# Performance work log

Measured on AMD Instinct MI355X. Metric: run time of the kernel, lower is better.

The kernel has to match this reference:

```python
import jax, jax.numpy as jnp
import numpy as np

L, H = 3, 8
B, N, D, E = 4, 256, 128, 128
NH, EH1, EH2 = 512, 512, 512


def _ln(x, g, b):
    m = x.mean(-1, keepdims=True)
    v = ((x - m) ** 2).mean(-1, keepdims=True)
    return (x - m) * jax.lax.rsqrt(v + 1e-5) * g + b


def setup_inputs() -> dict:
    key = jax.random.key(0)
    ks = jax.random.split(key, 16)
    w = lambda k, *s: jax.random.normal(k, s, jnp.float32) * 0.02
    inp = {
        'node_features': jax.random.normal(ks[0], (B, N, D), jnp.float32),
        'edge_features': jax.random.normal(ks[1], (B, N, N, E), jnp.float32),
        'Wqkv_n': w(ks[2], L, D, 3 * D), 'bqkv_n': jnp.zeros((L, 3 * D)),
        'Wqkv_e': w(ks[3], L, E, 3 * D), 'bqkv_e': jnp.zeros((L, 3 * D)),
        'Wo': w(ks[4], L, D, D), 'bo': jnp.zeros((L, D)),
        'Wn1': w(ks[5], L, D, NH), 'bn1': jnp.zeros((L, NH)),
        'Wn2': w(ks[6], L, NH, D), 'bn2': jnp.zeros((L, D)),
        'ln1n_g': jnp.ones((L, D)), 'ln1n_b': jnp.zeros((L, D)),
        'ln2n_g': jnp.ones((L, D)), 'ln2n_b': jnp.zeros((L, D)),
        'We1a': w(ks[7], L, 2 * D + 2 * E, EH1), 'be1a': jnp.zeros((L, EH1)),
        'We1b': w(ks[8], L, EH1, E), 'be1b': jnp.zeros((L, E)),
        'We2a': w(ks[9], L, E, EH2), 'be2a': jnp.zeros((L, EH2)),
        'We2b': w(ks[10], L, EH2, E), 'be2b': jnp.zeros((L, E)),
        'ln1e_g': jnp.ones((L, E)), 'ln1e_b': jnp.zeros((L, E)),
        'ln2e_g': jnp.ones((L, E)), 'ln2e_b': jnp.zeros((L, E)),
    }
    return inp


def reference(node_features, edge_features, Wqkv_n, bqkv_n, Wqkv_e, bqkv_e, Wo, bo,
              Wn1, bn1, Wn2, bn2, ln1n_g, ln1n_b, ln2n_g, ln2n_b,
              We1a, be1a, We1b, be1b, We2a, be2a, We2b, be2b,
              ln1e_g, ln1e_b, ln2e_g, ln2e_b):
    n, e = node_features, edge_features
    b_, N_, D_ = n.shape
    hd = D_ // H
    scale = 1.0 / np.sqrt(hd).astype(np.float32)
    for l in range(Wqkv_n.shape[0]):
        # ---- edge-biased attention ----
        qkv_n = (n @ Wqkv_n[l] + bqkv_n[l]).reshape(b_, N_, H, 3 * hd).transpose(0, 2, 1, 3)  # B,H,N,3hd
        q_n, k_n, v_n = jnp.split(qkv_n, 3, axis=-1)
        qkv_e = (e @ Wqkv_e[l] + bqkv_e[l]).reshape(b_, N_, N_, H, 3 * hd).transpose(0, 3, 1, 2, 4)  # B,H,N,N,3hd
        q_e, k_e, v_e = jnp.split(qkv_e, 3, axis=-1)
        q = q_n[:, :, :, None, :] + q_e  # B,H,N,N,hd
        # NOTE: the original torch code overwrites k with q (`k = q.reshape(...)`),
        # so scores are the squared norm of q; k_n/k_e are dead code. Faithful.
        scores = jnp.einsum('bhijd,bhijd->bhij', q, q) * scale
        att = jax.nn.softmax(scores, axis=-1)
        v = v_n[:, :, None, :, :] + v_e  # B,H,N,N,hd
        out = jnp.einsum('bhij,bhijd->bhid', att, v)  # B,H,N,hd
        out = out.transpose(0, 2, 1, 3).reshape(b_, N_, D_) @ Wo[l] + bo[l]
        n = _ln(n + out, ln1n_g[l], ln1n_b[l])
        ff = jax.nn.relu(n @ Wn1[l] + bn1[l]) @ Wn2[l] + bn2[l]
        n = _ln(n + ff, ln2n_g[l], ln2n_b[l])
        # ---- edge update ----
        src = jnp.broadcast_to(n[:, None, :, :], (b_, N_, N_, D_))  # node j
        tgt = jnp.broadcast_to(n[:, :, None, :], (b_, N_, N_, D_))  # node i
        cat = jnp.concatenate([e, e.transpose(0, 2, 1, 3), src, tgt], axis=-1)
        e1 = jax.nn.relu(cat @ We1a[l] + be1a[l]) @ We1b[l] + be1b[l]
        e = _ln(e + e1, ln1e_g[l], ln1e_b[l])
        e2 = jax.nn.relu(e @ We2a[l] + be2a[l]) @ We2b[l] + be2b[l]
        e = _ln(e + e2, ln2e_g[l], ln2e_b[l])
    return n
```

## Files before the change

kernel.cpp:

```cpp
#include <hip/hip_runtime.h>

typedef unsigned short u16;
typedef __bf16 bf16x8 __attribute__((ext_vector_type(8)));
typedef float f32x4 __attribute__((ext_vector_type(4)));

#define NB 4
#define NN 256
#define DD 128
#define RNN 262144

__device__ __forceinline__ u16 f2b(float f) {
    unsigned u = __builtin_bit_cast(unsigned, f);
    unsigned rb = ((u >> 16) & 1u) + 0x7FFFu;
    return (u16)((u + rb) >> 16);
}
__device__ __forceinline__ float b2f(u16 u) {
    return __builtin_bit_cast(float, ((unsigned)u) << 16);
}

__device__ __forceinline__ void glds16(const void* g, void* l) {
    __builtin_amdgcn_global_load_lds((const __attribute__((address_space(1))) void*)g,
                                     (__attribute__((address_space(3))) void*)l, 16, 0, 0);
}

__global__ void prep_weights(const float* __restrict__ Wqkv_e, const float* __restrict__ bqkv_e,
                             const float* __restrict__ We1a, const float* __restrict__ We1b,
                             const float* __restrict__ We2a, const float* __restrict__ We2b,
                             u16* wqT, u16* wv, float* bqp, float* bvp,
                             u16* we1aT, u16* we1bT, u16* we2aT, u16* we2bT) {
    int l = blockIdx.z, sec = blockIdx.y;
    int idx = blockIdx.x * 256 + threadIdx.x;
    if (sec == 0) {
        if (idx < 16384) {
            int n = idx >> 7, k = idx & 127;
            int col = (n >> 4) * 48 + (n & 15);
            wqT[l * 16384 + n * 128 + k] = f2b(Wqkv_e[l * 49152 + k * 384 + col]);
        }
    } else if (sec == 1) {
        if (idx < 16384) {
            int k = idx >> 7, c = idx & 127;
            int col = (c >> 4) * 48 + 32 + (c & 15);
            wv[l * 16384 + k * 128 + c] = f2b(Wqkv_e[l * 49152 + k * 384 + col]);
        }
        if (idx < 128) {
            bqp[l * 128 + idx] = bqkv_e[l * 384 + (idx >> 4) * 48 + (idx & 15)];
            bvp[l * 128 + idx] = bqkv_e[l * 384 + (idx >> 4) * 48 + 32 + (idx & 15)];
        }
    } else if (sec == 2) {
        if (idx < 131072) {
            int n = idx >> 8, k = idx & 255;
            we1aT[l * 131072 + n * 256 + k] = f2b(We1a[l * 262144 + k * 512 + n]);
        }
    } else if (sec == 3) {
        if (idx < 65536) {
            int n = idx >> 9, k = idx & 511;
            we1bT[l * 65536 + n * 512 + k] = f2b(We1b[l * 65536 + k * 128 + n]);
        }
    } else if (sec == 4) {
        if (idx < 65536) {
            int n = idx >> 7, k = idx & 127;
            we2aT[l * 65536 + n * 128 + k] = f2b(We2a[l * 65536 + k * 512 + n]);
        }
    } else {
        if (idx < 65536) {
            int n = idx >> 9, k = idx & 511;
            we2bT[l * 65536 + n * 512 + k] = f2b(We2b[l * 65536 + k * 128 + n]);
        }
    }
}

__global__ void init_e(const float4* __restrict__ src, ushort4* __restrict__ dst) {
    const long n4 = 8388608;
    for (long i = (long)blockIdx.x * blockDim.x + threadIdx.x; i < n4; i += (long)gridDim.x * blockDim.x) {
        float4 v = src[i];
        ushort4 o;
        o.x = f2b(v.x); o.y = f2b(v.y); o.z = f2b(v.z); o.w = f2b(v.w);
        dst[i] = o;
    }
}

__global__ void init_n(const float* __restrict__ node, float* __restrict__ nf) {
    int i = blockIdx.x * 256 + threadIdx.x;
    if (i < 131072) nf[i] = node[i];
}

__launch_bounds__(512)
__global__ void pre_node_kernel(const float* __restrict__ nf, const float* __restrict__ We1a,
                                float* __restrict__ preS, float* __restrict__ preT) {
    __shared__ float nr[128];
    int tid = threadIdx.x;
    int row = blockIdx.x;
    if (tid < 128) nr[tid] = nf[(long)row * 128 + tid];
    __syncthreads();
    int c = tid;
    float s = 0.f, t = 0.f;
    const float* Ws = We1a + (long)256 * 512 + c;
    const float* Wt = We1a + (long)384 * 512 + c;
    #pragma unroll 8
    for (int k = 0; k < 128; ++k) {
        float nv = nr[k];
        s += nv * Ws[k * 512];
        t += nv * Wt[k * 512];
    }
    preS[(long)row * 512 + c] = s;
    preT[(long)row * 512 + c] = t;
}

__global__ void qkvn_kernel(const float* __restrict__ nf, const float* __restrict__ W,
                            const float* __restrict__ bias, float* __restrict__ qn, float* __restrict__ vn) {
    __shared__ float nr[128];
    int tid = threadIdx.x;
    int row = blockIdx.x;
    if (tid < 128) nr[tid] = nf[(long)row * 128 + tid];
    __syncthreads();
    int c = tid & 127;
    bool isq = tid < 128;
    int col = (c >> 4) * 48 + (c & 15) + (isq ? 0 : 32);
    float a = bias[col];
    #pragma unroll 8
    for (int k = 0; k < 128; ++k) a += nr[k] * W[k * 384 + col];
    if (isq) qn[(long)row * 128 + c] = a;
    else     vn[(long)row * 128 + c] = a;
}

__launch_bounds__(256, 2)
__global__ void scores_kernel(const u16* __restrict__ ein, const u16* __restrict__ WqT,
                              const float* __restrict__ bqp, const float* __restrict__ qn,
                              float* __restrict__ scoresp) {
    __shared__ u16 As[128 * 64];
    __shared__ u16 Bs[128 * 64];
    int tid = threadIdx.x;
    int wid = tid >> 6, lane = tid & 63;
    int bid = blockIdx.x;
    int jhalf = bid & 1, bi = bid >> 1;
    int b = bi >> 8, i = bi & 255;
    int wr = wid >> 1, wc = wid & 1;

    f32x4 acc[4][4];
    f32x4 z = {0.f, 0.f, 0.f, 0.f};
    #pragma unroll
    for (int m = 0; m < 4; ++m)
        #pragma unroll
        for (int n = 0; n < 4; ++n) acc[m][n] = z;

    const long arow0 = ((long)(b * NN + i) * NN + jhalf * 128);
    for (int kt = 0; kt < 2; ++kt) {
        int k0 = kt << 6;
        #pragma unroll
        for (int p = 0; p < 4; ++p) {
            int r = p * 32 + (tid >> 3);
            int ch = tid & 7;
            const u16* src = ein + (arow0 + r) * 128 + k0 + ((ch ^ (r & 7)) << 3);
            glds16(src, (char*)As + (p << 12) + (wid << 10));
            int n = p * 32 + (tid >> 3);
            const u16* bsrc = WqT + (long)n * 128 + k0 + ((ch ^ (n & 7)) << 3);
            glds16(bsrc, (char*)Bs + (p << 12) + (wid << 10));
        }
        __syncthreads();
        #pragma unroll
        for (int ks = 0; ks < 2; ++ks) {
            bf16x8 af[4], bfr[4];
            #pragma unroll
            for (int m = 0; m < 4; ++m) {
                int r = wr * 64 + m * 16 + (lane & 15);
                int ch = (ks * 4 + (lane >> 4)) ^ (r & 7);
                af[m] = *reinterpret_cast<const bf16x8*>(&As[r * 64 + ch * 8]);
            }
            #pragma unroll
            for (int n = 0; n < 4; ++n) {
                int c = wc * 64 + n * 16 + (lane & 15);
                int ch = (ks * 4 + (lane >> 4)) ^ (c & 7);
                bfr[n] = *reinterpret_cast<const bf16x8*>(&Bs[c * 64 + ch * 8]);
            }
            #pragma unroll
            for (int m = 0; m < 4; ++m)
                #pragma unroll
                for (int n = 0; n < 4; ++n)
                    acc[m][n] = __builtin_amdgcn_mfma_f32_16x16x32_bf16(af[m], bfr[n], acc[m][n], 0, 0, 0);
        }
        __syncthreads();
    }
    const float* qnb = qn + (long)(b * NN + i) * 128;
    #pragma unroll
    for (int m = 0; m < 4; ++m) {
        #pragma unroll
        for (int n = 0; n < 4; ++n) {
            int col = wc * 64 + n * 16 + (lane & 15);
            float add = bqp[col] + qnb[col];
            float sv[4];
            #pragma unroll
            for (int t = 0; t < 4; ++t) { float qv = acc[m][n][t] + add; sv[t] = qv * qv; }
            #pragma unroll
            for (int mk = 1; mk <= 8; mk <<= 1)
                #pragma unroll
                for (int t = 0; t < 4; ++t) sv[t] += __shfl_xor(sv[t], mk);
            if ((lane & 15) == 0) {
                int head = wc * 4 + n;
                int jb = jhalf * 128 + wr * 64 + m * 16 + ((lane >> 4) << 2);
                long sbase = ((long)(b * 8 + head) * 256 + i) * 256 + jb;
                #pragma unroll
                for (int t = 0; t < 4; ++t) scoresp[sbase + t] = sv[t] * 0.25f;
            }
        }
    }
}

__launch_bounds__(256)
__global__ void attn_pv_kernel(const float* __restrict__ scoresp, const u16* __restrict__ ein,
                               const float* __restrict__ vn, const u16* __restrict__ Wv,
                               const float* __restrict__ bvp, float* __restrict__ attn_o) {
    __shared__ float s_s[8 * 256];
    __shared__ float g_s[8 * 128];
    __shared__ float part[256];
    int tid = threadIdx.x;
    int b = blockIdx.x >> 8, i = blockIdx.x & 255;
    for (int v = tid; v < 2048; v += 256) {
        int h = v >> 8, j = v & 255;
        s_s[v] = scoresp[((long)(b * 8 + h) * 256 + i) * 256 + j];
    }
    __syncthreads();
    {
        int h = tid >> 5, lg = tid & 31;
        float vals[8], mx = -1e30f;
        #pragma unroll
        for (int t = 0; t < 8; ++t) { vals[t] = s_s[h * 256 + lg + t * 32]; mx = fmaxf(mx, vals[t]); }
        #pragma unroll
        for (int mk = 16; mk; mk >>= 1) mx = fmaxf(mx, __shfl_xor(mx, mk));
        float sum = 0.f;
        #pragma unroll
        for (int t = 0; t < 8; ++t) { vals[t] = __expf(vals[t] - mx); sum += vals[t]; }
        #pragma unroll
        for (int mk = 16; mk; mk >>= 1) sum += __shfl_xor(sum, mk);
        float inv = 1.f / sum;
        #pragma unroll
        for (int t = 0; t < 8; ++t) s_s[h * 256 + lg + t * 32] = vals[t] * inv;
    }
    __syncthreads();
    {
        int k = tid & 127, h0 = tid >> 7;
        const u16* erow = ein + ((long)(b * NN + i) * NN) * 128 + k;
        float a0 = 0, a1 = 0, a2 = 0, a3 = 0;
        for (int j = 0; j < 256; ++j) {
            float ev = b2f(erow[(long)j * 128]);
            a0 += s_s[(h0    ) * 256 + j] * ev;
            a1 += s_s[(h0 + 2) * 256 + j] * ev;
            a2 += s_s[(h0 + 4) * 256 + j] * ev;
            a3 += s_s[(h0 + 6) * 256 + j] * ev;
        }
        g_s[(h0    ) * 128 + k] = a0;
        g_s[(h0 + 2) * 128 + k] = a1;
        g_s[(h0 + 4) * 128 + k] = a2;
        g_s[(h0 + 6) * 128 + k] = a3;
    }
    __syncthreads();
    {
        int c = tid & 127, half = tid >> 7;
        int h = c >> 4;
        float a = 0.f;
        for (int j = half * 128; j < half * 128 + 128; ++j)
            a += s_s[h * 256 + j] * vn[((long)(b * NN + j)) * 128 + c];
        for (int k = half * 64; k < half * 64 + 64; ++k)
            a += g_s[h * 128 + k] * b2f(Wv[k * 128 + c]);
        part[tid] = a;
    }
    __syncthreads();
    if (tid < 128)
        attn_o[((long)(b * NN + i)) * 128 + tid] = part[tid] + part[128 + tid] + bvp[tid];
}

__launch_bounds__(256)
__global__ void node_kernel(const float* __restrict__ attn_o, float* __restrict__ nf,
                            const float* __restrict__ Wo, const float* __restrict__ bo,
                            const float* __restrict__ Wn1, const float* __restrict__ bn1,
                            const float* __restrict__ Wn2, const float* __restrict__ bn2,
                            const float* __restrict__ g1, const float* __restrict__ b1,
                            const float* __restrict__ g2, const float* __restrict__ b2) {
    __shared__ float ao[128], nr[128], n1[128], hb[512];
    __shared__ float red[8];
    int tid = threadIdx.x;
    int wid = tid >> 6, lane = tid & 63;
    long base = (long)blockIdx.x * 128;
    if (tid < 128) { ao[tid] = attn_o[base + tid]; nr[tid] = nf[base + tid]; }
    __syncthreads();
    float x = 0.f;
    if (tid < 128) {
        float a = bo[tid];
        #pragma unroll 8
        for (int k = 0; k < 128; ++k) a += ao[k] * Wo[k * 128 + tid];
        x = nr[tid] + a;
    }
    float s = (tid < 128) ? x : 0.f, q = (tid < 128) ? x * x : 0.f;
    #pragma unroll
    for (int mk = 1; mk <= 32; mk <<= 1) { s += __shfl_xor(s, mk); q += __shfl_xor(q, mk); }
    if (lane == 0) { red[wid * 2] = s; red[wid * 2 + 1] = q; }
    __syncthreads();
    float sum = red[0] + red[2] + red[4] + red[6];
    float sq  = red[1] + red[3] + red[5] + red[7];
    float mean = sum * (1.f / 128.f);
    float var = sq * (1.f / 128.f) - mean * mean;
    float rs = rsqrtf(var + 1e-5f);
    __syncthreads();
    if (tid < 128) n1[tid] = (x - mean) * rs * g1[tid] + b1[tid];
    __syncthreads();
    for (int c = tid; c < 512; c += 256) {
        float a = bn1[c];
        #pragma unroll 8
        for (int k = 0; k < 128; ++k) a += n1[k] * Wn1[k * 512 + c];
        hb[c] = a > 0.f ? a : 0.f;
    }
    __syncthreads();
    float y = 0.f;
    if (tid < 128) {
        float a = bn2[tid];
        #pragma unroll 8
        for (int k = 0; k < 512; ++k) a += hb[k] * Wn2[k * 128 + tid];
        y = n1[tid] + a;
    }
    float s2 = (tid < 128) ? y : 0.f, q2 = (tid < 128) ? y * y : 0.f;
    #pragma unroll
    for (int mk = 1; mk <= 32; mk <<= 1) { s2 += __shfl_xor(s2, mk); q2 += __shfl_xor(q2, mk); }
    if (lane == 0) { red[wid * 2] = s2; red[wid * 2 + 1] = q2; }
    __syncthreads();
    sum = red[0] + red[2] + red[4] + red[6];
    sq  = red[1] + red[3] + red[5] + red[7];
    mean = sum * (1.f / 128.f);
    var = sq * (1.f / 128.f) - mean * mean;
    rs = rsqrtf(var + 1e-5f);
    if (tid < 128) {
        float o = (y - mean) * rs * g2[tid] + b2[tid];
        nf[base + tid] = o;
    }
}

template<int KT1, int CAT>
__launch_bounds__(256, 2)
__global__ void fused_mlp4(const u16* __restrict__ W1T, const float* __restrict__ b1v,
                           const u16* __restrict__ W2T, const float* __restrict__ b2v,
                           const u16* __restrict__ ein, const u16* __restrict__ Aplain,
                           const float* __restrict__ preS, const float* __restrict__ preT,
                           const float* __restrict__ lng, const float* __restrict__ lnb,
                           u16* __restrict__ e_dst) {
    __shared__ __align__(16) u16 A_lds[KT1 * 4096];
    __shared__ __align__(16) u16 Wsl[2][8192];
    __shared__ __align__(16) u16 Hs[8192];

    constexpr int K1 = KT1 * 64;
    int tid = threadIdx.x;
    int wid = tid >> 6, lane = tid & 63;
    long row0 = (long)blockIdx.x * 64;
    int b = (int)(row0 >> 16);
    int rem0 = (int)(row0 & 65535);
    int i_ = rem0 >> 8, j0 = rem0 & 255;
    int wn = wid >> 1, wrr = wid & 1;
    int wr2 = wid >> 1, wc2 = wid & 1;

    auto stageW1 = [&](int qq, int kt, int slot) {
        char* dst = (char*)Wsl[slot];
        #pragma unroll
        for (int pp = 0; pp < 4; ++pp) {
            int nl = pp * 32 + (tid >> 3);
            int ch = tid & 7;
            const u16* src = W1T + (long)((qq << 7) + nl) * K1 + (kt << 6) + ((ch ^ (nl & 7)) << 3);
            glds16(src, dst + (pp << 12) + (wid << 10));
        }
    };
    auto stageW2 = [&](int qq, int kt2, int slot) {
        char* dst = (char*)Wsl[slot];
        #pragma unroll
        for (int pp = 0; pp < 4; ++pp) {
            int cl = pp * 32 + (tid >> 3);
            int ch = tid & 7;
            const u16* src = W2T + (long)cl * 512 + (qq << 7) + (kt2 << 6) + ((ch ^ (cl & 7)) << 3);
            glds16(src, dst + (pp << 12) + (wid << 10));
        }
    };

    f32x4 z = {0.f, 0.f, 0.f, 0.f};
    f32x4 acc2[2][4];
    #pragma unroll
    for (int m = 0; m < 2; ++m)
        #pragma unroll
        for (int n = 0; n < 4; ++n) acc2[m][n] = z;

    #pragma unroll
    for (int kt = 0; kt < KT1; ++kt)
        #pragma unroll
        for (int pp = 0; pp < 2; ++pp) {
            int r = pp * 32 + (tid >> 3);
            int ch = tid & 7;
            const u16* src;
            if constexpr (CAT) {
                long ridx = (kt < 2) ? (long)(b * NN + i_) * NN + (j0 + r)
                                     : (long)(b * NN + (j0 + r)) * NN + i_;
                src = ein + ridx * DD + ((kt & 1) << 6) + ((ch ^ (r & 7)) << 3);
            } else {
                src = Aplain + (row0 + r) * K1 + (kt << 6) + ((ch ^ (r & 7)) << 3);
            }
            glds16(src, (char*)A_lds + kt * 8192 + (pp << 12) + (wid << 10));
        }
    stageW1(0, 0, 0);

    for (int q = 0; q < 4; ++q) {
        f32x4 acc1[4][2];
        #pragma unroll
        for (int mn = 0; mn < 4; ++mn) { acc1[mn][0] = z; acc1[mn][1] = z; }

        #pragma unroll
        for (int kt = 0; kt < KT1; ++kt) {
            __builtin_amdgcn_s_barrier();
            __builtin_amdgcn_sched_barrier(0);
            if (kt + 1 < KT1) stageW1(q, kt + 1, (kt + 1) & 1);
            else              stageW2(q, 0, (kt + 1) & 1);
            __builtin_amdgcn_sched_barrier(0);
            asm volatile("s_waitcnt vmcnt(4)" ::: "memory");
            __builtin_amdgcn_sched_barrier(0);
            const u16* w = Wsl[kt & 1];
            __builtin_amdgcn_s_setprio(1);
            #pragma unroll
            for (int ks = 0; ks < 2; ++ks) {
                bf16x8 af[4], bfr[2];
                #pragma unroll
                for (int mn = 0; mn < 4; ++mn) {
                    int n = wn * 64 + mn * 16 + (lane & 15);
                    int ch = (ks * 4 + (lane >> 4)) ^ (n & 7);
                    af[mn] = *reinterpret_cast<const bf16x8*>(&w[n * 64 + ch * 8]);
                }
                #pragma unroll
                for (int mr = 0; mr < 2; ++mr) {
                    int r = wrr * 32 + mr * 16 + (lane & 15);
                    int ch = (ks * 4 + (lane >> 4)) ^ (r & 7);
                    bfr[mr] = *reinterpret_cast<const bf16x8*>(&A_lds[kt * 4096 + r * 64 + ch * 8]);
                }
                #pragma unroll
                for (int mn = 0; mn < 4; ++mn)
                    #pragma unroll
                    for (int mr = 0; mr < 2; ++mr)
                        acc1[mn][mr] = __builtin_amdgcn_mfma_f32_16x16x32_bf16(af[mn], bfr[mr], acc1[mn][mr], 0, 0, 0);
            }
            __builtin_amdgcn_s_setprio(0);
        }

        #pragma unroll
        for (int mn = 0; mn < 4; ++mn) {
            int nl0 = wn * 64 + mn * 16 + ((lane >> 4) << 2);
            int n0g = (q << 7) + nl0;
            float4 bb = *reinterpret_cast<const float4*>(&b1v[n0g]);
            if constexpr (CAT) {
                float4 pt = *reinterpret_cast<const float4*>(&preT[(long)(b * NN + i_) * 512 + n0g]);
                bb.x += pt.x; bb.y += pt.y; bb.z += pt.z; bb.w += pt.w;
            }
            #pragma unroll
            for (int mr = 0; mr < 2; ++mr) {
                int r = wrr * 32 + mr * 16 + (lane & 15);
                float b0 = bb.x, b1_ = bb.y, b2_ = bb.z, b3 = bb.w;
                if constexpr (CAT) {
                    float4 ps = *reinterpret_cast<const float4*>(&preS[(long)(b * NN + j0 + r) * 512 + n0g]);
                    b0 += ps.x; b1_ += ps.y; b2_ += ps.z; b3 += ps.w;
                }
                float v0 = acc1[mn][mr][0] + b0; v0 = v0 > 0.f ? v0 : 0.f;
                float v1 = acc1[mn][mr][1] + b1_; v1 = v1 > 0.f ? v1 : 0.f;
                float v2 = acc1[mn][mr][2] + b2_; v2 = v2 > 0.f ? v2 : 0.f;
                float v3 = acc1[mn][mr][3] + b3; v3 = v3 > 0.f ? v3 : 0.f;
                uint2 pk;
                pk.x = (unsigned)f2b(v0) | ((unsigned)f2b(v1) << 16);
                pk.y = (unsigned)f2b(v2) | ((unsigned)f2b(v3) << 16);
                int c8 = nl0 >> 3;
                int cs = (c8 & 8) | ((c8 ^ r) & 7);
                *reinterpret_cast<uint2*>((char*)Hs + r * 256 + cs * 16 + (nl0 & 7) * 2) = pk;
            }
        }
        asm volatile("s_waitcnt lgkmcnt(0)" ::: "memory");

        #pragma unroll
        for (int kt2 = 0; kt2 < 2; ++kt2) {
            __builtin_amdgcn_s_barrier();
            __builtin_amdgcn_sched_barrier(0);
            if (kt2 == 0)      stageW2(q, 1, 1);
            else if (q < 3)    stageW1(q + 1, 0, 0);
            __builtin_amdgcn_sched_barrier(0);
            if (kt2 == 0 || q < 3) asm volatile("s_waitcnt vmcnt(4)" ::: "memory");
            else                   asm volatile("s_waitcnt vmcnt(0)" ::: "memory");
            __builtin_amdgcn_sched_barrier(0);
            const u16* w = Wsl[kt2 & 1];
            __builtin_amdgcn_s_setprio(1);
            #pragma unroll
            for (int ks = 0; ks < 2; ++ks) {
                bf16x8 af2[2], bf2[4];
                #pragma unroll
                for (int m = 0; m < 2; ++m) {
                    int r = wr2 * 32 + m * 16 + (lane & 15);
                    int lk = kt2 * 64 + ks * 32 + ((lane >> 4) << 3);
                    int c8 = lk >> 3;
                    int cs = (c8 & 8) | ((c8 ^ r) & 7);
                    af2[m] = *reinterpret_cast<const bf16x8*>((const char*)Hs + r * 256 + cs * 16);
                }
                #pragma unroll
                for (int n = 0; n < 4; ++n) {
                    int c = wc2 * 64 + n * 16 + (lane & 15);
                    int chn = (ks * 4 + (lane >> 4)) ^ (c & 7);
                    bf2[n] = *reinterpret_cast<const bf16x8*>(&w[c * 64 + chn * 8]);
                }
                #pragma unroll
                for (int m = 0; m < 2; ++m)
                    #pragma unroll
                    for (int n = 0; n < 4; ++n)
                        acc2[m][n] = __builtin_amdgcn_mfma_f32_16x16x32_bf16(af2[m], bf2[n], acc2[m][n], 0, 0, 0);
            }
            __builtin_amdgcn_s_setprio(0);
        }
    }
    __syncthreads();

    float* psum = (float*)Hs;
    float* psq  = psum + 128;
    #pragma unroll
    for (int m = 0; m < 2; ++m) {
        float sv[4] = {0.f, 0.f, 0.f, 0.f}, qv[4] = {0.f, 0.f, 0.f, 0.f};
        #pragma unroll
        for (int n = 0; n < 4; ++n) {
            int col = wc2 * 64 + n * 16 + (lane & 15);
            float bb = b2v[col];
            int kk = col & 63, kreg = col >> 6;
            #pragma unroll
            for (int t = 0; t < 4; ++t) {
                int row = wr2 * 32 + m * 16 + ((lane >> 4) << 2) + t;
                float er = b2f(A_lds[kreg * 4096 + row * 64 + (((kk >> 3) ^ (row & 7)) << 3) + (kk & 7)]);
                float x = acc2[m][n][t] + bb + er;
                acc2[m][n][t] = x;
                sv[t] += x;
                qv[t] += x * x;
            }
        }
        #pragma unroll
        for (int mk = 1; mk <= 8; mk <<= 1)
            #pragma unroll
            for (int t = 0; t < 4; ++t) { sv[t] += __shfl_xor(sv[t], mk); qv[t] += __shfl_xor(qv[t], mk); }
        if ((lane & 15) == 0) {
            #pragma unroll
            for (int t = 0; t < 4; ++t) {
                int row = wr2 * 32 + m * 16 + ((lane >> 4) << 2) + t;
                psum[row * 2 + wc2] = sv[t];
                psq[row * 2 + wc2] = qv[t];
            }
        }
    }
    __syncthreads();
    u16* rp;
    if constexpr (KT1 == 4) rp = A_lds + 8192;
    else                    rp = Wsl[0];
    #pragma unroll
    for (int m = 0; m < 2; ++m) {
        #pragma unroll
        for (int t = 0; t < 4; ++t) {
            int row = wr2 * 32 + m * 16 + ((lane >> 4) << 2) + t;
            float sum = psum[row * 2] + psum[row * 2 + 1];
            float sq  = psq[row * 2] + psq[row * 2 + 1];
            float mean = sum * (1.f / 128.f);
            float var = sq * (1.f / 128.f) - mean * mean;
            float rs = rsqrtf(var + 1e-5f);
            #pragma unroll
            for (int n = 0; n < 4; ++n) {
                int col = wc2 * 64 + n * 16 + (lane & 15);
                float o = (acc2[m][n][t] - mean) * rs * lng[col] + lnb[col];
                rp[row * 128 + col] = f2b(o);
            }
        }
    }
    __syncthreads();
    #pragma unroll
    for (int pp = 0; pp < 4; ++pp) {
        ulonglong2 v = *reinterpret_cast<const ulonglong2*>((char*)rp + (pp << 12) + tid * 16);
        *reinterpret_cast<ulonglong2*>((char*)e_dst + row0 * 256 + (pp << 12) + tid * 16) = v;
    }
}

extern "C" void kernel_launch(void* const* d_in, const int* in_sizes, int n_in,
                              void* d_out, int out_size, void* d_ws, size_t ws_size,
                              hipStream_t stream) {
    (void)in_sizes; (void)n_in; (void)out_size; (void)ws_size;
    const float* node   = (const float*)d_in[0];
    const float* edge   = (const float*)d_in[1];
    const float* Wqkv_n = (const float*)d_in[2];
    const float* bqkv_n = (const float*)d_in[3];
    const float* Wqkv_e = (const float*)d_in[4];
    const float* bqkv_e = (const float*)d_in[5];
    const float* Wo     = (const float*)d_in[6];
    const float* bo     = (const float*)d_in[7];
    const float* Wn1    = (const float*)d_in[8];
    const float* bn1    = (const float*)d_in[9];
    const float* Wn2    = (const float*)d_in[10];
    const float* bn2    = (const float*)d_in[11];
    const float* ln1n_g = (const float*)d_in[12];
    const float* ln1n_b = (const float*)d_in[13];
    const float* ln2n_g = (const float*)d_in[14];
    const float* ln2n_b = (const float*)d_in[15];
    const float* We1a   = (const float*)d_in[16];
    const float* be1a   = (const float*)d_in[17];
    const float* We1b   = (const float*)d_in[18];
    const float* be1b   = (const float*)d_in[19];
    const float* We2a   = (const float*)d_in[20];
    const float* be2a   = (const float*)d_in[21];
    const float* We2b   = (const float*)d_in[22];
    const float* be2b   = (const float*)d_in[23];
    const float* ln1e_g = (const float*)d_in[24];
    const float* ln1e_b = (const float*)d_in[25];
    const float* ln2e_g = (const float*)d_in[26];
    const float* ln2e_b = (const float*)d_in[27];

    size_t off = 0;
    char* wsb = (char*)d_ws;
    auto alloc = [&](size_t bytes) -> void* {
        void* p = wsb + off;
        off = (off + bytes + 255) & ~(size_t)255;
        return p;
    };
    u16* eb0      = (u16*)alloc((size_t)RNN * 128 * 2);
    u16* eb1      = (u16*)alloc((size_t)RNN * 128 * 2);
    float* scoresp= (float*)alloc((size_t)2097152 * 4);
    float* qn     = (float*)alloc(131072 * 4);
    float* vn     = (float*)alloc(131072 * 4);
    float* attn_o = (float*)alloc(131072 * 4);
    float* nf     = (float*)alloc(131072 * 4);
    float* preS   = (float*)alloc((size_t)1024 * 512 * 4);
    float* preT   = (float*)alloc((size_t)1024 * 512 * 4);
    u16* wqT      = (u16*)alloc(3 * 16384 * 2);
    u16* wv       = (u16*)alloc(3 * 16384 * 2);
    float* bqp    = (float*)alloc(3 * 128 * 4);
    float* bvp    = (float*)alloc(3 * 128 * 4);
    u16* we1aT    = (u16*)alloc(3 * 131072ull * 2);
    u16* we1bT    = (u16*)alloc(3 * 65536 * 2);
    u16* we2aT    = (u16*)alloc(3 * 65536 * 2);
    u16* we2bT    = (u16*)alloc(3 * 65536 * 2);

    {
        dim3 g(1024, 6, 3);
        prep_weights<<<g, 256, 0, stream>>>(Wqkv_e, bqkv_e, We1a, We1b, We2a, We2b,
                                            wqT, wv, bqp, bvp, we1aT, we1bT, we2aT, we2bT);
    }
    init_e<<<2048, 256, 0, stream>>>((const float4*)edge, (ushort4*)eb0);
    init_n<<<512, 256, 0, stream>>>(node, nf);

    for (int l = 0; l < 3; ++l) {
        u16* ein  = (l & 1) ? eb1 : eb0;
        u16* eout = (l & 1) ? eb0 : eb1;
        qkvn_kernel<<<1024, 256, 0, stream>>>(nf, Wqkv_n + l * 49152, bqkv_n + l * 384, qn, vn);
        scores_kernel<<<2048, 256, 0, stream>>>(ein, wqT + l * 16384, bqp + l * 128, qn, scoresp);
        attn_pv_kernel<<<1024, 256, 0, stream>>>(scoresp, ein, vn, wv + l * 16384, bvp + l * 128, attn_o);
        node_kernel<<<1024, 256, 0, stream>>>(attn_o, nf,
                                              Wo + l * 16384, bo + l * 128,
                                              Wn1 + l * 65536, bn1 + l * 512,
                                              Wn2 + l * 65536, bn2 + l * 128,
                                              ln1n_g + l * 128, ln1n_b + l * 128,
                                              ln2n_g + l * 128, ln2n_b + l * 128);
        pre_node_kernel<<<1024, 512, 0, stream>>>(nf, We1a + (size_t)l * 262144, preS, preT);
        fused_mlp4<4, 1><<<4096, 256, 0, stream>>>(we1aT + l * 131072, be1a + l * 512,
                                                   we1bT + l * 65536, be1b + l * 128,
                                                   ein, nullptr, preS, preT,
                                                   ln1e_g + l * 128, ln1e_b + l * 128, eout);
        fused_mlp4<2, 0><<<4096, 256, 0, stream>>>(we2aT + l * 65536, be2a + l * 512,
                                                   we2bT + l * 65536, be2b + l * 128,
                                                   nullptr, eout, nullptr, nullptr,
                                                   ln2e_g + l * 128, ln2e_b + l * 128, eout);
    }
    hipMemcpyAsync(d_out, nf, 131072 * sizeof(float), hipMemcpyDeviceToDevice, stream);
}
```

Baseline: 1.521 ms.

## Load MFMA weight fragments directly from global in pre-swizzled layout

The weight prep now writes the edge-MLP weights in a fragment-ordered layout, so each lane can load its MFMA operand with one 16-byte global load. The weight LDS double buffer and its staging are removed. Warps are re-split so each owns a slice of output columns across all 64 rows, and the LayerNorm reduction now goes through a small dedicated shared array. Lower LDS use lets launch bounds rise to 3 blocks per CU, trading LDS staging for register-prefetched global (L2-cached) weight reads.

Measured after the change: 1.322 ms. 13.1% less time.

```diff
diff --git a/kernel.cpp b/kernel.cpp
--- a/kernel.cpp
+++ b/kernel.cpp
@@ -27,7 +27,7 @@
                              const float* __restrict__ We1a, const float* __restrict__ We1b,
                              const float* __restrict__ We2a, const float* __restrict__ We2b,
                              u16* wqT, u16* wv, float* bqp, float* bvp,
-                             u16* we1aT, u16* we1bT, u16* we2aT, u16* we2bT) {
+                             u16* w1f_e1, u16* w2f_e1, u16* w1f_e2, u16* w2f_e2) {
     int l = blockIdx.z, sec = blockIdx.y;
     int idx = blockIdx.x * 256 + threadIdx.x;
     if (sec == 0) {
@@ -48,23 +48,39 @@
         }
     } else if (sec == 2) {
         if (idx < 131072) {
-            int n = idx >> 8, k = idx & 255;
-            we1aT[l * 131072 + n * 256 + k] = f2b(We1a[l * 262144 + k * 512 + n]);
+            int step = idx >> 13, q = step >> 2, kt = step & 3;
+            int rem = idx & 8191;
+            int nb = rem >> 10, ks = (rem >> 9) & 1, ln = (rem >> 3) & 63, j = rem & 7;
+            int n = q * 128 + nb * 16 + (ln & 15);
+            int k = kt * 64 + ks * 32 + (ln >> 4) * 8 + j;
+            w1f_e1[l * 131072 + idx] = f2b(We1a[l * 262144 + k * 512 + n]);
         }
     } else if (sec == 3) {
         if (idx < 65536) {
-            int n = idx >> 9, k = idx & 511;
-            we1bT[l * 65536 + n * 512 + k] = f2b(We1b[l * 65536 + k * 128 + n]);
+            int step = idx >> 13, q = step >> 1, kt2 = step & 1;
+            int rem = idx & 8191;
+            int cb = rem >> 10, ks = (rem >> 9) & 1, ln = (rem >> 3) & 63, j = rem & 7;
+            int c = cb * 16 + (ln & 15);
+            int k = q * 128 + kt2 * 64 + ks * 32 + (ln >> 4) * 8 + j;
+            w2f_e1[l * 65536 + idx] = f2b(We1b[l * 65536 + k * 128 + c]);
         }
     } else if (sec == 4) {
         if (idx < 65536) {
-            int n = idx >> 7, k = idx & 127;
-            we2aT[l * 65536 + n * 128 + k] = f2b(We2a[l * 65536 + k * 512 + n]);
+            int step = idx >> 13, q = step >> 1, kt = step & 1;
+            int rem = idx & 8191;
+            int nb = rem >> 10, ks = (rem >> 9) & 1, ln = (rem >> 3) & 63, j = rem & 7;
+            int n = q * 128 + nb * 16 + (ln & 15);
+            int k = kt * 64 + ks * 32 + (ln >> 4) * 8 + j;
+            w1f_e2[l * 65536 + idx] = f2b(We2a[l * 65536 + k * 512 + n]);
         }
     } else {
         if (idx < 65536) {
-            int n = idx >> 9, k = idx & 511;
-            we2bT[l * 65536 + n * 512 + k] = f2b(We2b[l * 65536 + k * 128 + n]);
+            int step = idx >> 13, q = step >> 1, kt2 = step & 1;
+            int rem = idx & 8191;
+            int cb = rem >> 10, ks = (rem >> 9) & 1, ln = (rem >> 3) & 63, j = rem & 7;
+            int c = cb * 16 + (ln & 15);
+            int k = q * 128 + kt2 * 64 + ks * 32 + (ln >> 4) * 8 + j;
+            w2f_e2[l * 65536 + idx] = f2b(We2b[l * 65536 + k * 128 + c]);
         }
     }
 }
@@ -333,16 +349,16 @@
 }
 
 template<int KT1, int CAT>
-__launch_bounds__(256, 2)
-__global__ void fused_mlp4(const u16* __restrict__ W1T, const float* __restrict__ b1v,
-                           const u16* __restrict__ W2T, const float* __restrict__ b2v,
+__launch_bounds__(256, 3)
+__global__ void fused_mlp5(const u16* __restrict__ W1F, const float* __restrict__ b1v,
+                           const u16* __restrict__ W2F, const float* __restrict__ b2v,
                            const u16* __restrict__ ein, const u16* __restrict__ Aplain,
                            const float* __restrict__ preS, const float* __restrict__ preT,
                            const float* __restrict__ lng, const float* __restrict__ lnb,
                            u16* __restrict__ e_dst) {
     __shared__ __align__(16) u16 A_lds[KT1 * 4096];
-    __shared__ __align__(16) u16 Wsl[2][8192];
     __shared__ __align__(16) u16 Hs[8192];
+    __shared__ float psum[256], psq[256];
 
     constexpr int K1 = KT1 * 64;
     int tid = threadIdx.x;
@@ -351,36 +367,6 @@
     int b = (int)(row0 >> 16);
     int rem0 = (int)(row0 & 65535);
     int i_ = rem0 >> 8, j0 = rem0 & 255;
-    int wn = wid >> 1, wrr = wid & 1;
-    int wr2 = wid >> 1, wc2 = wid & 1;
-
-    auto stageW1 = [&](int qq, int kt, int slot) {
-        char* dst = (char*)Wsl[slot];
-        #pragma unroll
-        for (int pp = 0; pp < 4; ++pp) {
-            int nl = pp * 32 + (tid >> 3);
-            int ch = tid & 7;
-            const u16* src = W1T + (long)((qq << 7) + nl) * K1 + (kt << 6) + ((ch ^ (nl & 7)) << 3);
-            glds16(src, dst + (pp << 12) + (wid << 10));
-        }
-    };
-    auto stageW2 = [&](int qq, int kt2, int slot) {
-        char* dst = (char*)Wsl[slot];
-        #pragma unroll
-        for (int pp = 0; pp < 4; ++pp) {
-            int cl = pp * 32 + (tid >> 3);
-            int ch = tid & 7;
-            const u16* src = W2T + (long)cl * 512 + (qq << 7) + (kt2 << 6) + ((ch ^ (cl & 7)) << 3);
-            glds16(src, dst + (pp << 12) + (wid << 10));
-        }
-    };
-
-    f32x4 z = {0.f, 0.f, 0.f, 0.f};
-    f32x4 acc2[2][4];
-    #pragma unroll
-    for (int m = 0; m < 2; ++m)
-        #pragma unroll
-        for (int n = 0; n < 4; ++n) acc2[m][n] = z;
 
     #pragma unroll
     for (int kt = 0; kt < KT1; ++kt)
@@ -398,51 +384,97 @@
             }
             glds16(src, (char*)A_lds + kt * 8192 + (pp << 12) + (wid << 10));
         }
-    stageW1(0, 0, 0);
-
+    asm volatile("s_waitcnt vmcnt(0)" ::: "memory");
+    __builtin_amdgcn_sched_barrier(0);
+    __builtin_amdgcn_s_barrier();
+    __builtin_amdgcn_sched_barrier(0);
+
+    const u16* w1base = W1F + (wid * 2) * 1024 + lane * 8;
+    const u16* w2base = W2F + (wid * 2) * 1024 + lane * 8;
+
+    f32x4 z = {0.f, 0.f, 0.f, 0.f};
+    f32x4 acc1[2][4], acc2[4][2];
+    #pragma unroll
+    for (int a = 0; a < 4; ++a) { acc2[a][0] = z; acc2[a][1] = z; }
+
+    bf16x8 afA[4], afB[4], g2A[4], g2B[4];
+
+    auto AFLD = [&](bf16x8 (&d)[4], int q, int kt) {
+        const u16* p = w1base + ((q * KT1 + kt) << 13);
+        d[0] = *reinterpret_cast<const bf16x8*>(p);
+        d[1] = *reinterpret_cast<const bf16x8*>(p + 1024);
+        d[2] = *reinterpret_cast<const bf16x8*>(p + 512);
+        d[3] = *reinterpret_cast<const bf16x8*>(p + 1536);
+    };
+    auto BFLD = [&](bf16x8 (&d)[4], int q, int kt2) {
+        const u16* p = w2base + ((q * 2 + kt2) << 13);
+        d[0] = *reinterpret_cast<const bf16x8*>(p);
+        d[1] = *reinterpret_cast<const bf16x8*>(p + 1024);
+        d[2] = *reinterpret_cast<const bf16x8*>(p + 512);
+        d[3] = *reinterpret_cast<const bf16x8*>(p + 1536);
+    };
+    auto G1K = [&](bf16x8 (&cur)[4], int kt) {
+        #pragma unroll
+        for (int ks = 0; ks < 2; ++ks) {
+            bf16x8 bfr[4];
+            #pragma unroll
+            for (int rf = 0; rf < 4; ++rf) {
+                int r = rf * 16 + (lane & 15);
+                int ch = (ks * 4 + (lane >> 4)) ^ (r & 7);
+                bfr[rf] = *reinterpret_cast<const bf16x8*>(&A_lds[kt * 4096 + r * 64 + ch * 8]);
+            }
+            #pragma unroll
+            for (int mn = 0; mn < 2; ++mn)
+                #pragma unroll
+                for (int rf = 0; rf < 4; ++rf)
+                    acc1[mn][rf] = __builtin_amdgcn_mfma_f32_16x16x32_bf16(cur[ks * 2 + mn], bfr[rf], acc1[mn][rf], 0, 0, 0);
+        }
+    };
+    auto G2K = [&](bf16x8 (&w)[4], int kt2) {
+        #pragma unroll
+        for (int ks = 0; ks < 2; ++ks) {
+            bf16x8 af2[4];
+            #pragma unroll
+            for (int rf = 0; rf < 4; ++rf) {
+                int r = rf * 16 + (lane & 15);
+                int c8 = kt2 * 8 + ks * 4 + (lane >> 4);
+                int cs = (c8 & 8) | ((c8 ^ r) & 7);
+                af2[rf] = *reinterpret_cast<const bf16x8*>((const char*)Hs + r * 256 + cs * 16);
+            }
+            #pragma unroll
+            for (int rf = 0; rf < 4; ++rf)
+                #pragma unroll
+                for (int cf = 0; cf < 2; ++cf)
+                    acc2[rf][cf] = __builtin_amdgcn_mfma_f32_16x16x32_bf16(af2[rf], w[ks * 2 + cf], acc2[rf][cf], 0, 0, 0);
+        }
+    };
+
+    AFLD(afA, 0, 0);
     for (int q = 0; q < 4; ++q) {
-        f32x4 acc1[4][2];
-        #pragma unroll
-        for (int mn = 0; mn < 4; ++mn) { acc1[mn][0] = z; acc1[mn][1] = z; }
-
-        #pragma unroll
-        for (int kt = 0; kt < KT1; ++kt) {
+        #pragma unroll
+        for (int mn = 0; mn < 2; ++mn)
+            #pragma unroll
+            for (int rf = 0; rf < 4; ++rf) acc1[mn][rf] = z;
+
+        if constexpr (KT1 == 4) {
+            AFLD(afB, q, 1); G1K(afA, 0);
+            AFLD(afA, q, 2); G1K(afB, 1);
+            AFLD(afB, q, 3); G1K(afA, 2);
+            G1K(afB, 3);
+        } else {
+            AFLD(afB, q, 1); G1K(afA, 0);
+            G1K(afB, 1);
+        }
+
+        BFLD(g2A, q, 0);
+        if (q) {
+            __builtin_amdgcn_sched_barrier(0);
             __builtin_amdgcn_s_barrier();
             __builtin_amdgcn_sched_barrier(0);
-            if (kt + 1 < KT1) stageW1(q, kt + 1, (kt + 1) & 1);
-            else              stageW2(q, 0, (kt + 1) & 1);
-            __builtin_amdgcn_sched_barrier(0);
-            asm volatile("s_waitcnt vmcnt(4)" ::: "memory");
-            __builtin_amdgcn_sched_barrier(0);
-            const u16* w = Wsl[kt & 1];
-            __builtin_amdgcn_s_setprio(1);
-            #pragma unroll
-            for (int ks = 0; ks < 2; ++ks) {
-                bf16x8 af[4], bfr[2];
-                #pragma unroll
-                for (int mn = 0; mn < 4; ++mn) {
-                    int n = wn * 64 + mn * 16 + (lane & 15);
-                    int ch = (ks * 4 + (lane >> 4)) ^ (n & 7);
-                    af[mn] = *reinterpret_cast<const bf16x8*>(&w[n * 64 + ch * 8]);
-                }
-                #pragma unroll
-                for (int mr = 0; mr < 2; ++mr) {
-                    int r = wrr * 32 + mr * 16 + (lane & 15);
-                    int ch = (ks * 4 + (lane >> 4)) ^ (r & 7);
-                    bfr[mr] = *reinterpret_cast<const bf16x8*>(&A_lds[kt * 4096 + r * 64 + ch * 8]);
-                }
-                #pragma unroll
-                for (int mn = 0; mn < 4; ++mn)
-                    #pragma unroll
-                    for (int mr = 0; mr < 2; ++mr)
-                        acc1[mn][mr] = __builtin_amdgcn_mfma_f32_16x16x32_bf16(af[mn], bfr[mr], acc1[mn][mr], 0, 0, 0);
-            }
-            __builtin_amdgcn_s_setprio(0);
-        }
-
-        #pragma unroll
-        for (int mn = 0; mn < 4; ++mn) {
-            int nl0 = wn * 64 + mn * 16 + ((lane >> 4) << 2);
+        }
+        #pragma unroll
+        for (int mn = 0; mn < 2; ++mn) {
+            int nl0 = wid * 32 + mn * 16 + ((lane >> 4) << 2);
             int n0g = (q << 7) + nl0;
             float4 bb = *reinterpret_cast<const float4*>(&b1v[n0g]);
             if constexpr (CAT) {
@@ -450,17 +482,17 @@
                 bb.x += pt.x; bb.y += pt.y; bb.z += pt.z; bb.w += pt.w;
             }
             #pragma unroll
-            for (int mr = 0; mr < 2; ++mr) {
-                int r = wrr * 32 + mr * 16 + (lane & 15);
+            for (int rf = 0; rf < 4; ++rf) {
+                int r = rf * 16 + (lane & 15);
                 float b0 = bb.x, b1_ = bb.y, b2_ = bb.z, b3 = bb.w;
                 if constexpr (CAT) {
                     float4 ps = *reinterpret_cast<const float4*>(&preS[(long)(b * NN + j0 + r) * 512 + n0g]);
                     b0 += ps.x; b1_ += ps.y; b2_ += ps.z; b3 += ps.w;
                 }
-                float v0 = acc1[mn][mr][0] + b0; v0 = v0 > 0.f ? v0 : 0.f;
-                float v1 = acc1[mn][mr][1] + b1_; v1 = v1 > 0.f ? v1 : 0.f;
-                float v2 = acc1[mn][mr][2] + b2_; v2 = v2 > 0.f ? v2 : 0.f;
-                float v3 = acc1[mn][mr][3] + b3; v3 = v3 > 0.f ? v3 : 0.f;
+                float v0 = acc1[mn][rf][0] + b0; v0 = v0 > 0.f ? v0 : 0.f;
+                float v1 = acc1[mn][rf][1] + b1_; v1 = v1 > 0.f ? v1 : 0.f;
+                float v2 = acc1[mn][rf][2] + b2_; v2 = v2 > 0.f ? v2 : 0.f;
+                float v3 = acc1[mn][rf][3] + b3; v3 = v3 > 0.f ? v3 : 0.f;
                 uint2 pk;
                 pk.x = (unsigned)f2b(v0) | ((unsigned)f2b(v1) << 16);
                 pk.y = (unsigned)f2b(v2) | ((unsigned)f2b(v3) << 16);
@@ -470,63 +502,30 @@
             }
         }
         asm volatile("s_waitcnt lgkmcnt(0)" ::: "memory");
-
-        #pragma unroll
-        for (int kt2 = 0; kt2 < 2; ++kt2) {
-            __builtin_amdgcn_s_barrier();
-            __builtin_amdgcn_sched_barrier(0);
-            if (kt2 == 0)      stageW2(q, 1, 1);
-            else if (q < 3)    stageW1(q + 1, 0, 0);
-            __builtin_amdgcn_sched_barrier(0);
-            if (kt2 == 0 || q < 3) asm volatile("s_waitcnt vmcnt(4)" ::: "memory");
-            else                   asm volatile("s_waitcnt vmcnt(0)" ::: "memory");
-            __builtin_amdgcn_sched_barrier(0);
-            const u16* w = Wsl[kt2 & 1];
-            __builtin_amdgcn_s_setprio(1);
-            #pragma unroll
-            for (int ks = 0; ks < 2; ++ks) {
-                bf16x8 af2[2], bf2[4];
-                #pragma unroll
-                for (int m = 0; m < 2; ++m) {
-                    int r = wr2 * 32 + m * 16 + (lane & 15);
-                    int lk = kt2 * 64 + ks * 32 + ((lane >> 4) << 3);
-                    int c8 = lk >> 3;
-                    int cs = (c8 & 8) | ((c8 ^ r) & 7);
-                    af2[m] = *reinterpret_cast<const bf16x8*>((const char*)Hs + r * 256 + cs * 16);
-                }
-                #pragma unroll
-                for (int n = 0; n < 4; ++n) {
-                    int c = wc2 * 64 + n * 16 + (lane & 15);
-                    int chn = (ks * 4 + (lane >> 4)) ^ (c & 7);
-                    bf2[n] = *reinterpret_cast<const bf16x8*>(&w[c * 64 + chn * 8]);
-                }
-                #pragma unroll
-                for (int m = 0; m < 2; ++m)
-                    #pragma unroll
-                    for (int n = 0; n < 4; ++n)
-                        acc2[m][n] = __builtin_amdgcn_mfma_f32_16x16x32_bf16(af2[m], bf2[n], acc2[m][n], 0, 0, 0);
-            }
-            __builtin_amdgcn_s_setprio(0);
-        }
-    }
-    __syncthreads();
-
-    float* psum = (float*)Hs;
-    float* psq  = psum + 128;
-    #pragma unroll
-    for (int m = 0; m < 2; ++m) {
+        __builtin_amdgcn_sched_barrier(0);
+        __builtin_amdgcn_s_barrier();
+        __builtin_amdgcn_sched_barrier(0);
+
+        BFLD(g2B, q, 1);
+        G2K(g2A, 0);
+        if (q < 3) AFLD(afA, q + 1, 0);
+        G2K(g2B, 1);
+    }
+
+    #pragma unroll
+    for (int rf = 0; rf < 4; ++rf) {
         float sv[4] = {0.f, 0.f, 0.f, 0.f}, qv[4] = {0.f, 0.f, 0.f, 0.f};
         #pragma unroll
-        for (int n = 0; n < 4; ++n) {
-            int col = wc2 * 64 + n * 16 + (lane & 15);
-            float bb = b2v[col];
-            int kk = col & 63, kreg = col >> 6;
+        for (int cf = 0; cf < 2; ++cf) {
+            int c = wid * 32 + cf * 16 + (lane & 15);
+            float bb = b2v[c];
+            int kk = c & 63, kreg = c >> 6;
             #pragma unroll
             for (int t = 0; t < 4; ++t) {
-                int row = wr2 * 32 + m * 16 + ((lane >> 4) << 2) + t;
-                float er = b2f(A_lds[kreg * 4096 + row * 64 + (((kk >> 3) ^ (row & 7)) << 3) + (kk & 7)]);
-                float x = acc2[m][n][t] + bb + er;
-                acc2[m][n][t] = x;
+                int r = rf * 16 + ((lane >> 4) << 2) + t;
+                float er = b2f(A_lds[kreg * 4096 + r * 64 + (((kk >> 3) ^ (r & 7)) << 3) + (kk & 7)]);
+                float x = acc2[rf][cf][t] + bb + er;
+                acc2[rf][cf][t] = x;
                 sv[t] += x;
                 qv[t] += x * x;
             }
@@ -538,38 +537,35 @@
         if ((lane & 15) == 0) {
             #pragma unroll
             for (int t = 0; t < 4; ++t) {
-                int row = wr2 * 32 + m * 16 + ((lane >> 4) << 2) + t;
-                psum[row * 2 + wc2] = sv[t];
-                psq[row * 2 + wc2] = qv[t];
-            }
-        }
-    }
-    __syncthreads();
-    u16* rp;
-    if constexpr (KT1 == 4) rp = A_lds + 8192;
-    else                    rp = Wsl[0];
-    #pragma unroll
-    for (int m = 0; m < 2; ++m) {
+                int r = rf * 16 + ((lane >> 4) << 2) + t;
+                psum[r * 4 + wid] = sv[t];
+                psq[r * 4 + wid] = qv[t];
+            }
+        }
+    }
+    __syncthreads();
+    #pragma unroll
+    for (int rf = 0; rf < 4; ++rf) {
         #pragma unroll
         for (int t = 0; t < 4; ++t) {
-            int row = wr2 * 32 + m * 16 + ((lane >> 4) << 2) + t;
-            float sum = psum[row * 2] + psum[row * 2 + 1];
-            float sq  = psq[row * 2] + psq[row * 2 + 1];
+            int r = rf * 16 + ((lane >> 4) << 2) + t;
+            float sum = psum[r * 4] + psum[r * 4 + 1] + psum[r * 4 + 2] + psum[r * 4 + 3];
+            float sq  = psq[r * 4] + psq[r * 4 + 1] + psq[r * 4 + 2] + psq[r * 4 + 3];
             float mean = sum * (1.f / 128.f);
             float var = sq * (1.f / 128.f) - mean * mean;
             float rs = rsqrtf(var + 1e-5f);
             #pragma unroll
-            for (int n = 0; n < 4; ++n) {
-                int col = wc2 * 64 + n * 16 + (lane & 15);
-                float o = (acc2[m][n][t] - mean) * rs * lng[col] + lnb[col];
-                rp[row * 128 + col] = f2b(o);
+            for (int cf = 0; cf < 2; ++cf) {
+                int c = wid * 32 + cf * 16 + (lane & 15);
+                float o = (acc2[rf][cf][t] - mean) * rs * lng[c] + lnb[c];
+                Hs[r * 128 + c] = f2b(o);
             }
         }
     }
     __syncthreads();
     #pragma unroll
     for (int pp = 0; pp < 4; ++pp) {
-        ulonglong2 v = *reinterpret_cast<const ulonglong2*>((char*)rp + (pp << 12) + tid * 16);
+        ulonglong2 v = *reinterpret_cast<const ulonglong2*>((char*)Hs + (pp << 12) + tid * 16);
         *reinterpret_cast<ulonglong2*>((char*)e_dst + row0 * 256 + (pp << 12) + tid * 16) = v;
     }
 }
@@ -627,15 +623,15 @@
     u16* wv       = (u16*)alloc(3 * 16384 * 2);
     float* bqp    = (float*)alloc(3 * 128 * 4);
     float* bvp    = (float*)alloc(3 * 128 * 4);
-    u16* we1aT    = (u16*)alloc(3 * 131072ull * 2);
-    u16* we1bT    = (u16*)alloc(3 * 65536 * 2);
-    u16* we2aT    = (u16*)alloc(3 * 65536 * 2);
-    u16* we2bT    = (u16*)alloc(3 * 65536 * 2);
+    u16* w1f_e1   = (u16*)alloc(3 * 131072ull * 2);
+    u16* w2f_e1   = (u16*)alloc(3 * 65536 * 2);
+    u16* w1f_e2   = (u16*)alloc(3 * 65536 * 2);
+    u16* w2f_e2   = (u16*)alloc(3 * 65536 * 2);
 
     {
-        dim3 g(1024, 6, 3);
+        dim3 g(512, 6, 3);
         prep_weights<<<g, 256, 0, stream>>>(Wqkv_e, bqkv_e, We1a, We1b, We2a, We2b,
-                                            wqT, wv, bqp, bvp, we1aT, we1bT, we2aT, we2bT);
+                                            wqT, wv, bqp, bvp, w1f_e1, w2f_e1, w1f_e2, w2f_e2);
     }
     init_e<<<2048, 256, 0, stream>>>((const float4*)edge, (ushort4*)eb0);
     init_n<<<512, 256, 0, stream>>>(node, nf);
@@ -653,12 +649,12 @@
                                               ln1n_g + l * 128, ln1n_b + l * 128,
                                               ln2n_g + l * 128, ln2n_b + l * 128);
         pre_node_kernel<<<1024, 512, 0, stream>>>(nf, We1a + (size_t)l * 262144, preS, preT);
-        fused_mlp4<4, 1><<<4096, 256, 0, stream>>>(we1aT + l * 131072, be1a + l * 512,
-                                                   we1bT + l * 65536, be1b + l * 128,
+        fused_mlp5<4, 1><<<4096, 256, 0, stream>>>(w1f_e1 + l * 131072, be1a + l * 512,
+                                                   w2f_e1 + l * 65536, be1b + l * 128,
                                                    ein, nullptr, preS, preT,
                                                    ln1e_g + l * 128, ln1e_b + l * 128, eout);
-        fused_mlp4<2, 0><<<4096, 256, 0, stream>>>(we2aT + l * 65536, be2a + l * 512,
-                                                   we2bT + l * 65536, be2b + l * 128,
+        fused_mlp5<2, 0><<<4096, 256, 0, stream>>>(w1f_e2 + l * 65536, be2a + l * 512,
+                                                   w2f_e2 + l * 65536, be2b + l * 128,
                                                    nullptr, eout, nullptr, nullptr,
                                                    ln2e_g + l * 128, ln2e_b + l * 128, eout);
     }
```
